# Optimization experiments

Measured on AMD Instinct MI355X. Metric: run time of the kernel, lower is better.

The kernel has to match this reference:

```python
import jax, jax.numpy as jnp
import numpy as np

B, S, D, H = 4, 2048, 1024, 16
HD = D // H

def rotate_half(x):
    x1, x2 = jnp.split(x, 2, axis=-1)
    return jnp.concatenate((-x2, x1), axis=-1)

def apply_rope(x, cos, sin):
    # x: [B,H,S,hd]; cos/sin: [S,hd] -> broadcast over B,H
    return x * cos[None, None] + rotate_half(x) * sin[None, None]

def setup_inputs() -> dict:
    key = jax.random.key(0)
    ks = jax.random.split(key, 8)
    x = jax.random.normal(ks[0], (B, S, D), dtype=jnp.float32)
    mask = jnp.triu(jnp.ones((S, S), dtype=bool), k=1)  # True = masked (causal)
    pos = jnp.arange(S, dtype=jnp.float32)[:, None]
    inv = 1.0 / (10000.0 ** (jnp.arange(0, HD, 2, dtype=jnp.float32) / HD))
    ang = pos * inv[None, :]  # [S, hd/2]
    ang = jnp.concatenate([ang, ang], axis=-1)  # [S, hd]
    rope_cos = jnp.cos(ang)
    rope_sin = jnp.sin(ang)
    scale = 1.0 / np.sqrt(D)
    Wq = jax.random.normal(ks[1], (D, D), dtype=jnp.float32) * scale
    Wk = jax.random.normal(ks[2], (D, D), dtype=jnp.float32) * scale
    Wv = jax.random.normal(ks[3], (D, D), dtype=jnp.float32) * scale
    Wo = jax.random.normal(ks[4], (D, D), dtype=jnp.float32) * scale
    z = jnp.zeros((D,), dtype=jnp.float32)
    return {"x": x, "mask": mask, "rope_cos": rope_cos, "rope_sin": rope_sin,
            "Wq": Wq, "bq": z, "Wk": Wk, "bk": z, "Wv": Wv, "bv": z, "Wo": Wo, "bo": z}

def reference(x, mask, rope_cos, rope_sin, Wq, bq, Wk, bk, Wv, bv, Wo, bo):
    b, s, d = x.shape
    def proj(W, bias):
        y = x @ W.T + bias  # torch Linear: x W^T + b
        return y.reshape(b, s, H, HD).transpose(0, 2, 1, 3)  # [B,H,S,hd]
    Q = apply_rope(proj(Wq, bq), rope_cos, rope_sin)
    K = apply_rope(proj(Wk, bk), rope_cos, rope_sin)
    V = proj(Wv, bv)
    scores = jnp.einsum('bhqd,bhkd->bhqk', Q, K) / jnp.sqrt(jnp.float32(HD))
    scores = jnp.where(mask[None, None], -jnp.inf, scores)
    attn = jax.nn.softmax(scores, axis=-1)
    ctx = jnp.einsum('bhqk,bhkd->bhqd', attn, V)
    ctx = ctx.transpose(0, 2, 1, 3).reshape(b, s, d)
    return ctx @ Wo.T + bo
```

## Files before the change

kernel.cpp:

```cpp
#include <hip/hip_runtime.h>
#include <hip/hip_bf16.h>

#define S_LEN 2048
#define D_MODEL 1024
#define NH 16
#define HDIM 64
#define B_SZ 4

typedef __attribute__((ext_vector_type(8))) short bf16x8;
typedef __attribute__((ext_vector_type(4))) float f32x4;

__device__ inline void gld16(const __hip_bfloat16* g, __hip_bfloat16* l) {
    __builtin_amdgcn_global_load_lds(
        (const __attribute__((address_space(1))) unsigned int*)g,
        (__attribute__((address_space(3))) unsigned int*)l, 16, 0, 0);
}

__device__ inline unsigned int pkbf(float a, float b) {
    float2 f; f.x = a; f.y = b;
    __hip_bfloat162 h = __float22bfloat162_rn(f);
    union { __hip_bfloat162 h; unsigned int u; } cv; cv.h = h; return cv.u;
}

__global__ __launch_bounds__(256) void f2bf4_kernel(const float4* __restrict__ in,
                                                    __hip_bfloat162* __restrict__ out,
                                                    int n4) {
    int i = blockIdx.x * 256 + threadIdx.x;
    if (i < n4) {
        float4 v = in[i];
        __hip_bfloat162 a, b;
        a.x = __float2bfloat16(v.x); a.y = __float2bfloat16(v.y);
        b.x = __float2bfloat16(v.z); b.y = __float2bfloat16(v.w);
        out[2 * i]     = a;
        out[2 * i + 1] = b;
    }
}

__global__ __launch_bounds__(256) void f2bfw_kernel(
    const float4* __restrict__ w0, const float4* __restrict__ w1,
    const float4* __restrict__ w2, const float4* __restrict__ w3,
    __hip_bfloat162* __restrict__ o0, __hip_bfloat162* __restrict__ o1,
    __hip_bfloat162* __restrict__ o2, __hip_bfloat162* __restrict__ o3) {
    const int z = blockIdx.y;
    const float4* in = (z == 0) ? w0 : (z == 1) ? w1 : (z == 2) ? w2 : w3;
    __hip_bfloat162* out = (z == 0) ? o0 : (z == 1) ? o1 : (z == 2) ? o2 : o3;
    int i = blockIdx.x * 256 + threadIdx.x;
    float4 v = in[i];
    __hip_bfloat162 a, b;
    a.x = __float2bfloat16(v.x); a.y = __float2bfloat16(v.y);
    b.x = __float2bfloat16(v.z); b.y = __float2bfloat16(v.w);
    out[2 * i]     = a;
    out[2 * i + 1] = b;
}

__device__ inline void gemm_mainloop(const __hip_bfloat16* __restrict__ X,
                                     const __hip_bfloat16* __restrict__ W,
                                     __hip_bfloat16* As, __hip_bfloat16* Bs,
                                     int m0, int n0, f32x4 acc[4][4]) {
    const int tid = threadIdx.x;
    const int wv = tid >> 6, lane = tid & 63, l15 = lane & 15, quad = lane >> 4;
    const int rw = (wv >> 1) * 64, cw = (wv & 1) * 64;
    for (int k0 = 0; k0 < D_MODEL; k0 += 32) {
        __syncthreads();
#pragma unroll
        for (int i = 0; i < 2; i++) {
            int l = tid + 256 * i;
            int row = l >> 2, c8 = (l & 3) * 8;
            gld16(&X[(size_t)(m0 + row) * D_MODEL + k0 + c8], &As[row * 32 + c8]);
            gld16(&W[(size_t)(n0 + row) * D_MODEL + k0 + c8], &Bs[row * 32 + c8]);
        }
        __syncthreads();
        bf16x8 af[4], bfr[4];
#pragma unroll
        for (int t = 0; t < 4; t++)
            af[t] = *(const bf16x8*)&As[(rw + t * 16 + l15) * 32 + quad * 8];
#pragma unroll
        for (int t = 0; t < 4; t++)
            bfr[t] = *(const bf16x8*)&Bs[(cw + t * 16 + l15) * 32 + quad * 8];
#pragma unroll
        for (int mt = 0; mt < 4; mt++)
#pragma unroll
            for (int nt = 0; nt < 4; nt++)
                acc[mt][nt] = __builtin_amdgcn_mfma_f32_16x16x32_bf16(
                    af[mt], bfr[nt], acc[mt][nt], 0, 0, 0);
    }
}

__global__ __launch_bounds__(256) void qkv_kernel(
    const __hip_bfloat16* __restrict__ X,
    const __hip_bfloat16* __restrict__ W0, const __hip_bfloat16* __restrict__ W1,
    const __hip_bfloat16* __restrict__ W2,
    const float* __restrict__ b0, const float* __restrict__ b1,
    const float* __restrict__ b2,
    const float* __restrict__ rc, const float* __restrict__ rs,
    __hip_bfloat16* __restrict__ Qo, __hip_bfloat16* __restrict__ Ko,
    __hip_bfloat16* __restrict__ Vo) {
    __shared__ __hip_bfloat16 As[128 * 32];
    __shared__ __hip_bfloat16 Bs[128 * 32];
    const int z = blockIdx.z;
    const __hip_bfloat16* W = (z == 0) ? W0 : ((z == 1) ? W1 : W2);
    const float* bias = (z == 0) ? b0 : ((z == 1) ? b1 : b2);
    f32x4 acc[4][4];
#pragma unroll
    for (int i = 0; i < 4; i++)
#pragma unroll
        for (int j = 0; j < 4; j++) acc[i][j] = (f32x4){0.f, 0.f, 0.f, 0.f};
    const int m0 = blockIdx.x * 128, n0 = blockIdx.y * 128;
    gemm_mainloop(X, W, As, Bs, m0, n0, acc);

    const int tid = threadIdx.x;
    const int wv = tid >> 6, lane = tid & 63, l15 = lane & 15, quad = lane >> 4;
    const int rw = (wv >> 1) * 64, cw = (wv & 1) * 64;

    if (z == 2) {
#pragma unroll
        for (int mt = 0; mt < 4; mt++)
#pragma unroll
            for (int r = 0; r < 4; r++) {
                int m = m0 + rw + mt * 16 + quad * 4 + r;
                int s = m & (S_LEN - 1), b = m >> 11;
#pragma unroll
                for (int nt = 0; nt < 4; nt++) {
                    int n = n0 + cw + nt * 16 + l15;
                    int h = n >> 6, hd = n & 63;
                    float v = acc[mt][nt][r] + bias[n];
                    Vo[(((size_t)(b * NH + h)) * S_LEN + s) * HDIM + hd] =
                        __float2bfloat16(v);
                }
            }
    } else {
        __hip_bfloat16* dst = (z == 0) ? Qo : Ko;
        const float qs = (z == 0) ? 0.18033688011112042f : 1.0f;
#pragma unroll
        for (int mt = 0; mt < 4; mt++)
#pragma unroll
            for (int r = 0; r < 4; r++) {
                int m = m0 + rw + mt * 16 + quad * 4 + r;
                int s = m & (S_LEN - 1), b = m >> 11;
#pragma unroll
                for (int nt = 0; nt < 2; nt++) {
                    int n1 = n0 + cw + nt * 16 + l15;
                    int h = n1 >> 6, hd1 = n1 & 63;
                    float y1 = acc[mt][nt][r] + bias[n1];
                    float y2 = acc[mt][nt + 2][r] + bias[n1 + 32];
                    float c1 = rc[s * HDIM + hd1], s1 = rs[s * HDIM + hd1];
                    float c2 = rc[s * HDIM + hd1 + 32], s2 = rs[s * HDIM + hd1 + 32];
                    size_t base = (((size_t)(b * NH + h)) * S_LEN + s) * HDIM;
                    dst[base + hd1]      = __float2bfloat16((y1 * c1 - y2 * s1) * qs);
                    dst[base + hd1 + 32] = __float2bfloat16((y2 * c2 + y1 * s2) * qs);
                }
            }
    }
}

#define KP 72
__global__ __launch_bounds__(256) void attn_kernel(
    const __hip_bfloat16* __restrict__ Q, const __hip_bfloat16* __restrict__ K,
    const __hip_bfloat16* __restrict__ V, __hip_bfloat16* __restrict__ CTX) {
    __shared__ __hip_bfloat16 Kl[2][64 * KP];
    __shared__ __hip_bfloat16 Vt[2][64 * KP];
    const int tid = threadIdx.x;
    const int wv = tid >> 6, lane = tid & 63, l15 = lane & 15, quad = lane >> 4;
    const int bh = blockIdx.x;
    const int pr = blockIdx.y;
    const int tA = pr, tC = 31 - pr;
    const int nkb = tC + 1;
    const size_t off = (size_t)bh * S_LEN * HDIM;
    const __hip_bfloat16* Qp = Q + off;
    const __hip_bfloat16* Kp = K + off;
    const __hip_bfloat16* Vp = V + off;

    bf16x8 qfA[2], qfC[2];
#pragma unroll
    for (int c = 0; c < 2; c++) {
        qfA[c] = *(const bf16x8*)&Qp[(size_t)(tA * 64 + wv * 16 + l15) * HDIM + c * 32 + quad * 8];
        qfC[c] = *(const bf16x8*)&Qp[(size_t)(tC * 64 + wv * 16 + l15) * HDIM + c * 32 + quad * 8];
    }

    float lA = 0.f, lC = 0.f;
    f32x4 accA[4], accC[4];
#pragma unroll
    for (int nt = 0; nt < 4; nt++) {
        accA[nt] = (f32x4){0.f, 0.f, 0.f, 0.f};
        accC[nt] = (f32x4){0.f, 0.f, 0.f, 0.f};
    }

    float4 kreg[2];
    unsigned short vreg[16];
    auto load_tile = [&](int kb) {
        const int k0 = kb * 64;
#pragma unroll
        for (int i = 0; i < 2; i++) {
            int l = tid + 256 * i;
            kreg[i] = *(const float4*)&Kp[(size_t)(k0 + (l >> 3)) * HDIM + (l & 7) * 8];
        }
#pragma unroll
        for (int j = 0; j < 16; j++)
            vreg[j] = *(const unsigned short*)&Vp[(size_t)(k0 + wv * 16 + j) * HDIM + lane];
    };
    auto store_tile = [&](int buf) {
#pragma unroll
        for (int i = 0; i < 2; i++) {
            int l = tid + 256 * i;
            *(float4*)&Kl[buf][(l >> 3) * KP + (l & 7) * 8] = kreg[i];
        }
        union { bf16x8 v; unsigned short u[8]; } p0, p1;
#pragma unroll
        for (int j = 0; j < 8; j++) { p0.u[j] = vreg[j]; p1.u[j] = vreg[8 + j]; }
        *(bf16x8*)&Vt[buf][lane * KP + wv * 16]     = p0.v;
        *(bf16x8*)&Vt[buf][lane * KP + wv * 16 + 8] = p1.v;
    };

    const int srcA = l15 + ((quad & 1) << 5);
    const int srcB = srcA + 16;
    const bool hi = (quad >> 1) != 0;
    const int qrel = wv * 16 + l15;

    load_tile(0);
    for (int kb = 0; kb < nkb; kb++) {
        const int buf = kb & 1;
        store_tile(buf);
        __syncthreads();
        if (kb + 1 < nkb) load_tile(kb + 1);

        const bool aAct = (kb <= tA);
        unsigned int pkC[8], pkA[8];

        {
            f32x4 sa[4];
#pragma unroll
            for (int st = 0; st < 4; st++) sa[st] = (f32x4){0.f, 0.f, 0.f, 0.f};
#pragma unroll
            for (int c = 0; c < 2; c++)
#pragma unroll
                for (int st = 0; st < 4; st++) {
                    bf16x8 kf = *(const bf16x8*)&Kl[buf][(st * 16 + l15) * KP + c * 32 + quad * 8];
                    sa[st] = __builtin_amdgcn_mfma_f32_16x16x32_bf16(kf, qfC[c], sa[st], 0, 0, 0);
                }
            float ls = 0.f;
            if (kb == tC) {
#pragma unroll
                for (int st = 0; st < 4; st++) {
                    float p[4];
#pragma unroll
                    for (int r = 0; r < 4; r++) {
                        bool msk = (st * 16 + quad * 4 + r > qrel);
                        p[r] = msk ? 0.f : __builtin_exp2f(sa[st][r]);
                        ls += p[r];
                    }
                    pkC[st * 2 + 0] = pkbf(p[0], p[1]);
                    pkC[st * 2 + 1] = pkbf(p[2], p[3]);
                }
            } else {
#pragma unroll
                for (int st = 0; st < 4; st++) {
                    float p[4];
#pragma unroll
                    for (int r = 0; r < 4; r++) {
                        p[r] = __builtin_exp2f(sa[st][r]);
                        ls += p[r];
                    }
                    pkC[st * 2 + 0] = pkbf(p[0], p[1]);
                    pkC[st * 2 + 1] = pkbf(p[2], p[3]);
                }
            }
            ls += __shfl_xor(ls, 16);
            ls += __shfl_xor(ls, 32);
            lC += ls;
        }
        if (aAct) {
            f32x4 sa[4];
#pragma unroll
            for (int st = 0; st < 4; st++) sa[st] = (f32x4){0.f, 0.f, 0.f, 0.f};
#pragma unroll
            for (int c = 0; c < 2; c++)
#pragma unroll
                for (int st = 0; st < 4; st++) {
                    bf16x8 kf = *(const bf16x8*)&Kl[buf][(st * 16 + l15) * KP + c * 32 + quad * 8];
                    sa[st] = __builtin_amdgcn_mfma_f32_16x16x32_bf16(kf, qfA[c], sa[st], 0, 0, 0);
                }
            float ls = 0.f;
            if (kb == tA) {
#pragma unroll
                for (int st = 0; st < 4; st++) {
                    float p[4];
#pragma unroll
                    for (int r = 0; r < 4; r++) {
                        bool msk = (st * 16 + quad * 4 + r > qrel);
                        p[r] = msk ? 0.f : __builtin_exp2f(sa[st][r]);
                        ls += p[r];
                    }
                    pkA[st * 2 + 0] = pkbf(p[0], p[1]);
                    pkA[st * 2 + 1] = pkbf(p[2], p[3]);
                }
            } else {
#pragma unroll
                for (int st = 0; st < 4; st++) {
                    float p[4];
#pragma unroll
                    for (int r = 0; r < 4; r++) {
                        p[r] = __builtin_exp2f(sa[st][r]);
                        ls += p[r];
                    }
                    pkA[st * 2 + 0] = pkbf(p[0], p[1]);
                    pkA[st * 2 + 1] = pkbf(p[2], p[3]);
                }
            }
            ls += __shfl_xor(ls, 16);
            ls += __shfl_xor(ls, 32);
            lA += ls;
        }

#pragma unroll
        for (int c = 0; c < 2; c++) {
            bf16x8 vf[4];
#pragma unroll
            for (int nt = 0; nt < 4; nt++)
                vf[nt] = *(const bf16x8*)&Vt[buf][(nt * 16 + l15) * KP + c * 32 + quad * 8];
            {
                unsigned int a0 = __shfl((int)pkC[4 * c + 0], srcA);
                unsigned int a1 = __shfl((int)pkC[4 * c + 1], srcA);
                unsigned int a2 = __shfl((int)pkC[4 * c + 0], srcB);
                unsigned int a3 = __shfl((int)pkC[4 * c + 1], srcB);
                unsigned int b0 = __shfl((int)pkC[4 * c + 2], srcA);
                unsigned int b1 = __shfl((int)pkC[4 * c + 3], srcA);
                unsigned int b2 = __shfl((int)pkC[4 * c + 2], srcB);
                unsigned int b3 = __shfl((int)pkC[4 * c + 3], srcB);
                union { unsigned int u[4]; bf16x8 v; } pf;
                pf.u[0] = hi ? b0 : a0;
                pf.u[1] = hi ? b1 : a1;
                pf.u[2] = hi ? b2 : a2;
                pf.u[3] = hi ? b3 : a3;
#pragma unroll
                for (int nt = 0; nt < 4; nt++)
                    accC[nt] = __builtin_amdgcn_mfma_f32_16x16x32_bf16(vf[nt], pf.v, accC[nt], 0, 0, 0);
            }
            if (aAct) {
                unsigned int a0 = __shfl((int)pkA[4 * c + 0], srcA);
                unsigned int a1 = __shfl((int)pkA[4 * c + 1], srcA);
                unsigned int a2 = __shfl((int)pkA[4 * c + 0], srcB);
                unsigned int a3 = __shfl((int)pkA[4 * c + 1], srcB);
                unsigned int b0 = __shfl((int)pkA[4 * c + 2], srcA);
                unsigned int b1 = __shfl((int)pkA[4 * c + 3], srcA);
                unsigned int b2 = __shfl((int)pkA[4 * c + 2], srcB);
                unsigned int b3 = __shfl((int)pkA[4 * c + 3], srcB);
                union { unsigned int u[4]; bf16x8 v; } pf;
                pf.u[0] = hi ? b0 : a0;
                pf.u[1] = hi ? b1 : a1;
                pf.u[2] = hi ? b2 : a2;
                pf.u[3] = hi ? b3 : a3;
#pragma unroll
                for (int nt = 0; nt < 4; nt++)
                    accA[nt] = __builtin_amdgcn_mfma_f32_16x16x32_bf16(vf[nt], pf.v, accA[nt], 0, 0, 0);
            }
        }
    }

    const int b = bh >> 4, h = bh & 15;
    {
        const int q = tA * 64 + wv * 16 + l15;
        const float inv = 1.0f / lA;
#pragma unroll
        for (int nt = 0; nt < 4; nt++) {
            uint2 st2;
            st2.x = pkbf(accA[nt][0] * inv, accA[nt][1] * inv);
            st2.y = pkbf(accA[nt][2] * inv, accA[nt][3] * inv);
            *(uint2*)&CTX[((size_t)(b * S_LEN + q)) * D_MODEL + h * HDIM + nt * 16 + quad * 4] = st2;
        }
    }
    {
        const int q = tC * 64 + wv * 16 + l15;
        const float inv = 1.0f / lC;
#pragma unroll
        for (int nt = 0; nt < 4; nt++) {
            uint2 st2;
            st2.x = pkbf(accC[nt][0] * inv, accC[nt][1] * inv);
            st2.y = pkbf(accC[nt][2] * inv, accC[nt][3] * inv);
            *(uint2*)&CTX[((size_t)(b * S_LEN + q)) * D_MODEL + h * HDIM + nt * 16 + quad * 4] = st2;
        }
    }
}

__global__ __launch_bounds__(256) void outproj_kernel(
    const __hip_bfloat16* __restrict__ X, const __hip_bfloat16* __restrict__ W,
    const float* __restrict__ bias, float* __restrict__ OUT) {
    __shared__ __hip_bfloat16 As[128 * 32];
    __shared__ __hip_bfloat16 Bs[128 * 32];
    f32x4 acc[4][4];
#pragma unroll
    for (int i = 0; i < 4; i++)
#pragma unroll
        for (int j = 0; j < 4; j++) acc[i][j] = (f32x4){0.f, 0.f, 0.f, 0.f};
    const int m0 = blockIdx.x * 128, n0 = blockIdx.y * 128;
    gemm_mainloop(X, W, As, Bs, m0, n0, acc);
    const int tid = threadIdx.x;
    const int wv = tid >> 6, lane = tid & 63, l15 = lane & 15, quad = lane >> 4;
    const int rw = (wv >> 1) * 64, cw = (wv & 1) * 64;
#pragma unroll
    for (int mt = 0; mt < 4; mt++)
#pragma unroll
        for (int r = 0; r < 4; r++) {
            int m = m0 + rw + mt * 16 + quad * 4 + r;
#pragma unroll
            for (int nt = 0; nt < 4; nt++) {
                int n = n0 + cw + nt * 16 + l15;
                OUT[(size_t)m * D_MODEL + n] = acc[mt][nt][r] + bias[n];
            }
        }
}

extern "C" void kernel_launch(void* const* d_in, const int* in_sizes, int n_in,
                              void* d_out, int out_size, void* d_ws, size_t ws_size,
                              hipStream_t stream) {
    const float* x  = (const float*)d_in[0];
    const float* rc = (const float*)d_in[2];
    const float* rs = (const float*)d_in[3];
    const float* Wq = (const float*)d_in[4];
    const float* bq = (const float*)d_in[5];
    const float* Wk = (const float*)d_in[6];
    const float* bk = (const float*)d_in[7];
    const float* Wv = (const float*)d_in[8];
    const float* bv = (const float*)d_in[9];
    const float* Wo = (const float*)d_in[10];
    const float* bo = (const float*)d_in[11];

    char* ws = (char*)d_ws;
    __hip_bfloat16* xbf = (__hip_bfloat16*)(ws);
    __hip_bfloat16* wqb = (__hip_bfloat16*)(ws + (16u << 20));
    __hip_bfloat16* wkb = (__hip_bfloat16*)(ws + (18u << 20));
    __hip_bfloat16* wvb = (__hip_bfloat16*)(ws + (20u << 20));
    __hip_bfloat16* wob = (__hip_bfloat16*)(ws + (22u << 20));
    __hip_bfloat16* Qb  = (__hip_bfloat16*)(ws + (24u << 20));
    __hip_bfloat16* Kb  = (__hip_bfloat16*)(ws + (40u << 20));
    __hip_bfloat16* Vb  = (__hip_bfloat16*)(ws + (56u << 20));
    __hip_bfloat16* Cb  = (__hip_bfloat16*)(ws + (72u << 20));
    float* out = (float*)d_out;

    f2bf4_kernel<<<8192, 256, 0, stream>>>((const float4*)x, (__hip_bfloat162*)xbf, 2097152);
    f2bfw_kernel<<<dim3(1024, 4), 256, 0, stream>>>(
        (const float4*)Wq, (const float4*)Wk, (const float4*)Wv, (const float4*)Wo,
        (__hip_bfloat162*)wqb, (__hip_bfloat162*)wkb, (__hip_bfloat162*)wvb,
        (__hip_bfloat162*)wob);

    qkv_kernel<<<dim3(64, 8, 3), 256, 0, stream>>>(xbf, wqb, wkb, wvb, bq, bk, bv,
                                                   rc, rs, Qb, Kb, Vb);
    attn_kernel<<<dim3(64, 16), 256, 0, stream>>>(Qb, Kb, Vb, Cb);
    outproj_kernel<<<dim3(64, 8), 256, 0, stream>>>(Cb, wob, bo, out);
}
```

Measured before the change: 341.2 us.

## Swizzle attention LDS tiles, stage P through LDS, single-buffer K/V

```diff
diff --git a/kernel.cpp b/kernel.cpp
--- a/kernel.cpp
+++ b/kernel.cpp
@@ -153,12 +153,13 @@
     }
 }
 
-#define KP 72
+#define SWZ(r, c) (((r) << 6) + ((c) ^ (((r) & 7) << 3)))
 __global__ __launch_bounds__(256) void attn_kernel(
     const __hip_bfloat16* __restrict__ Q, const __hip_bfloat16* __restrict__ K,
     const __hip_bfloat16* __restrict__ V, __hip_bfloat16* __restrict__ CTX) {
-    __shared__ __hip_bfloat16 Kl[2][64 * KP];
-    __shared__ __hip_bfloat16 Vt[2][64 * KP];
+    __shared__ __hip_bfloat16 Kl[64 * 64];
+    __shared__ __hip_bfloat16 Vt[64 * 64];
+    __shared__ __hip_bfloat16 Pl[2][4][16 * 64];
     const int tid = threadIdx.x;
     const int wv = tid >> 6, lane = tid & 63, l15 = lane & 15, quad = lane >> 4;
     const int bh = blockIdx.x;
@@ -169,6 +170,8 @@
     const __hip_bfloat16* Qp = Q + off;
     const __hip_bfloat16* Kp = K + off;
     const __hip_bfloat16* Vp = V + off;
+    __hip_bfloat16* PC = &Pl[0][wv][0];
+    __hip_bfloat16* PA = &Pl[1][wv][0];
 
     bf16x8 qfA[2], qfC[2];
 #pragma unroll
@@ -198,45 +201,57 @@
         for (int j = 0; j < 16; j++)
             vreg[j] = *(const unsigned short*)&Vp[(size_t)(k0 + wv * 16 + j) * HDIM + lane];
     };
-    auto store_tile = [&](int buf) {
+    auto store_tile = [&]() {
 #pragma unroll
         for (int i = 0; i < 2; i++) {
             int l = tid + 256 * i;
-            *(float4*)&Kl[buf][(l >> 3) * KP + (l & 7) * 8] = kreg[i];
+            *(float4*)&Kl[SWZ(l >> 3, (l & 7) * 8)] = kreg[i];
         }
         union { bf16x8 v; unsigned short u[8]; } p0, p1;
 #pragma unroll
         for (int j = 0; j < 8; j++) { p0.u[j] = vreg[j]; p1.u[j] = vreg[8 + j]; }
-        *(bf16x8*)&Vt[buf][lane * KP + wv * 16]     = p0.v;
-        *(bf16x8*)&Vt[buf][lane * KP + wv * 16 + 8] = p1.v;
+        *(bf16x8*)&Vt[SWZ(lane, wv * 16)]     = p0.v;
+        *(bf16x8*)&Vt[SWZ(lane, wv * 16 + 8)] = p1.v;
     };
 
-    const int srcA = l15 + ((quad & 1) << 5);
-    const int srcB = srcA + 16;
-    const bool hi = (quad >> 1) != 0;
     const int qrel = wv * 16 + l15;
 
     load_tile(0);
     for (int kb = 0; kb < nkb; kb++) {
-        const int buf = kb & 1;
-        store_tile(buf);
+        __syncthreads();
+        store_tile();
         __syncthreads();
         if (kb + 1 < nkb) load_tile(kb + 1);
 
         const bool aAct = (kb <= tA);
         unsigned int pkC[8], pkA[8];
 
+        f32x4 saC[4], saA[4];
+#pragma unroll
+        for (int st = 0; st < 4; st++) {
+            saC[st] = (f32x4){0.f, 0.f, 0.f, 0.f};
+            saA[st] = (f32x4){0.f, 0.f, 0.f, 0.f};
+        }
+        if (aAct) {
+#pragma unroll
+            for (int c = 0; c < 2; c++)
+#pragma unroll
+                for (int st = 0; st < 4; st++) {
+                    bf16x8 kf = *(const bf16x8*)&Kl[SWZ(st * 16 + l15, c * 32 + quad * 8)];
+                    saC[st] = __builtin_amdgcn_mfma_f32_16x16x32_bf16(kf, qfC[c], saC[st], 0, 0, 0);
+                    saA[st] = __builtin_amdgcn_mfma_f32_16x16x32_bf16(kf, qfA[c], saA[st], 0, 0, 0);
+                }
+        } else {
+#pragma unroll
+            for (int c = 0; c < 2; c++)
+#pragma unroll
+                for (int st = 0; st < 4; st++) {
+                    bf16x8 kf = *(const bf16x8*)&Kl[SWZ(st * 16 + l15, c * 32 + quad * 8)];
+                    saC[st] = __builtin_amdgcn_mfma_f32_16x16x32_bf16(kf, qfC[c], saC[st], 0, 0, 0);
+                }
+        }
+
         {
-            f32x4 sa[4];
-#pragma unroll
-            for (int st = 0; st < 4; st++) sa[st] = (f32x4){0.f, 0.f, 0.f, 0.f};
-#pragma unroll
-            for (int c = 0; c < 2; c++)
-#pragma unroll
-                for (int st = 0; st < 4; st++) {
-                    bf16x8 kf = *(const bf16x8*)&Kl[buf][(st * 16 + l15) * KP + c * 32 + quad * 8];
-                    sa[st] = __builtin_amdgcn_mfma_f32_16x16x32_bf16(kf, qfC[c], sa[st], 0, 0, 0);
-                }
             float ls = 0.f;
             if (kb == tC) {
 #pragma unroll
@@ -245,7 +260,7 @@
 #pragma unroll
                     for (int r = 0; r < 4; r++) {
                         bool msk = (st * 16 + quad * 4 + r > qrel);
-                        p[r] = msk ? 0.f : __builtin_exp2f(sa[st][r]);
+                        p[r] = msk ? 0.f : __builtin_exp2f(saC[st][r]);
                         ls += p[r];
                     }
                     pkC[st * 2 + 0] = pkbf(p[0], p[1]);
@@ -257,7 +272,7 @@
                     float p[4];
 #pragma unroll
                     for (int r = 0; r < 4; r++) {
-                        p[r] = __builtin_exp2f(sa[st][r]);
+                        p[r] = __builtin_exp2f(saC[st][r]);
                         ls += p[r];
                     }
                     pkC[st * 2 + 0] = pkbf(p[0], p[1]);
@@ -267,18 +282,13 @@
             ls += __shfl_xor(ls, 16);
             ls += __shfl_xor(ls, 32);
             lC += ls;
+#pragma unroll
+            for (int st = 0; st < 4; st++) {
+                uint2 w; w.x = pkC[st * 2]; w.y = pkC[st * 2 + 1];
+                *(uint2*)&PC[SWZ(l15, st * 16 + quad * 4)] = w;
+            }
         }
         if (aAct) {
-            f32x4 sa[4];
-#pragma unroll
-            for (int st = 0; st < 4; st++) sa[st] = (f32x4){0.f, 0.f, 0.f, 0.f};
-#pragma unroll
-            for (int c = 0; c < 2; c++)
-#pragma unroll
-                for (int st = 0; st < 4; st++) {
-                    bf16x8 kf = *(const bf16x8*)&Kl[buf][(st * 16 + l15) * KP + c * 32 + quad * 8];
-                    sa[st] = __builtin_amdgcn_mfma_f32_16x16x32_bf16(kf, qfA[c], sa[st], 0, 0, 0);
-                }
             float ls = 0.f;
             if (kb == tA) {
 #pragma unroll
@@ -287,7 +297,7 @@
 #pragma unroll
                     for (int r = 0; r < 4; r++) {
                         bool msk = (st * 16 + quad * 4 + r > qrel);
-                        p[r] = msk ? 0.f : __builtin_exp2f(sa[st][r]);
+                        p[r] = msk ? 0.f : __builtin_exp2f(saA[st][r]);
                         ls += p[r];
                     }
                     pkA[st * 2 + 0] = pkbf(p[0], p[1]);
@@ -299,7 +309,7 @@
                     float p[4];
 #pragma unroll
                     for (int r = 0; r < 4; r++) {
-                        p[r] = __builtin_exp2f(sa[st][r]);
+                        p[r] = __builtin_exp2f(saA[st][r]);
                         ls += p[r];
                     }
                     pkA[st * 2 + 0] = pkbf(p[0], p[1]);
@@ -309,6 +319,11 @@
             ls += __shfl_xor(ls, 16);
             ls += __shfl_xor(ls, 32);
             lA += ls;
+#pragma unroll
+            for (int st = 0; st < 4; st++) {
+                uint2 w; w.x = pkA[st * 2]; w.y = pkA[st * 2 + 1];
+                *(uint2*)&PA[SWZ(l15, st * 16 + quad * 4)] = w;
+            }
         }
 
 #pragma unroll
@@ -316,42 +331,18 @@
             bf16x8 vf[4];
 #pragma unroll
             for (int nt = 0; nt < 4; nt++)
-                vf[nt] = *(const bf16x8*)&Vt[buf][(nt * 16 + l15) * KP + c * 32 + quad * 8];
+                vf[nt] = *(const bf16x8*)&Vt[SWZ(nt * 16 + l15, c * 32 + quad * 8)];
             {
-                unsigned int a0 = __shfl((int)pkC[4 * c + 0], srcA);
-                unsigned int a1 = __shfl((int)pkC[4 * c + 1], srcA);
-                unsigned int a2 = __shfl((int)pkC[4 * c + 0], srcB);
-                unsigned int a3 = __shfl((int)pkC[4 * c + 1], srcB);
-                unsigned int b0 = __shfl((int)pkC[4 * c + 2], srcA);
-                unsigned int b1 = __shfl((int)pkC[4 * c + 3], srcA);
-                unsigned int b2 = __shfl((int)pkC[4 * c + 2], srcB);
-                unsigned int b3 = __shfl((int)pkC[4 * c + 3], srcB);
-                union { unsigned int u[4]; bf16x8 v; } pf;
-                pf.u[0] = hi ? b0 : a0;
-                pf.u[1] = hi ? b1 : a1;
-                pf.u[2] = hi ? b2 : a2;
-                pf.u[3] = hi ? b3 : a3;
+                bf16x8 pf = *(const bf16x8*)&PC[SWZ(l15, c * 32 + quad * 8)];
 #pragma unroll
                 for (int nt = 0; nt < 4; nt++)
-                    accC[nt] = __builtin_amdgcn_mfma_f32_16x16x32_bf16(vf[nt], pf.v, accC[nt], 0, 0, 0);
+                    accC[nt] = __builtin_amdgcn_mfma_f32_16x16x32_bf16(vf[nt], pf, accC[nt], 0, 0, 0);
             }
             if (aAct) {
-                unsigned int a0 = __shfl((int)pkA[4 * c + 0], srcA);
-                unsigned int a1 = __shfl((int)pkA[4 * c + 1], srcA);
-                unsigned int a2 = __shfl((int)pkA[4 * c + 0], srcB);
-                unsigned int a3 = __shfl((int)pkA[4 * c + 1], srcB);
-                unsigned int b0 = __shfl((int)pkA[4 * c + 2], srcA);
-                unsigned int b1 = __shfl((int)pkA[4 * c + 3], srcA);
-                unsigned int b2 = __shfl((int)pkA[4 * c + 2], srcB);
-                unsigned int b3 = __shfl((int)pkA[4 * c + 3], srcB);
-                union { unsigned int u[4]; bf16x8 v; } pf;
-                pf.u[0] = hi ? b0 : a0;
-                pf.u[1] = hi ? b1 : a1;
-                pf.u[2] = hi ? b2 : a2;
-                pf.u[3] = hi ? b3 : a3;
+                bf16x8 pf = *(const bf16x8*)&PA[SWZ(l15, c * 32 + quad * 8)];
 #pragma unroll
                 for (int nt = 0; nt < 4; nt++)
-                    accA[nt] = __builtin_amdgcn_mfma_f32_16x16x32_bf16(vf[nt], pf.v, accA[nt], 0, 0, 0);
+                    accA[nt] = __builtin_amdgcn_mfma_f32_16x16x32_bf16(vf[nt], pf, accA[nt], 0, 0, 0);
             }
         }
     }
```

After: 337.5 us. No clear change (-1.1%).
